# Optimization experiments

Hardware: AMD Instinct MI355X
Metric: run time of the kernel (lower is better)

The kernel has to match this reference:

```python
import jax, jax.numpy as jnp
import numpy as np

B, Q, F, D, H = 16384, 1024, 2, 5, 4  # batch, n_qubits, n_features, depth, heads


def setup_inputs() -> dict:
    key = jax.random.key(0)
    ks = iter(jax.random.split(key, 16))
    def rnd(shape, s=0.02):
        return jax.random.normal(next(ks), shape, dtype=jnp.float32) * s
    return {
        "x": jax.random.normal(next(ks), (B, F), dtype=jnp.float32),
        # amplitude_encoder: Linear(F,4Q) -> LN -> GELU -> Linear(4Q,2Q) -> LN -> Tanh -> Linear(2Q,Q)
        "amp_W1": rnd((4 * Q, F)), "amp_b1": jnp.zeros((4 * Q,), jnp.float32),
        "amp_g1": jnp.ones((4 * Q,), jnp.float32), "amp_be1": jnp.zeros((4 * Q,), jnp.float32),
        "amp_W2": rnd((2 * Q, 4 * Q)), "amp_b2": jnp.zeros((2 * Q,), jnp.float32),
        "amp_g2": jnp.ones((2 * Q,), jnp.float32), "amp_be2": jnp.zeros((2 * Q,), jnp.float32),
        "amp_W3": rnd((Q, 2 * Q)), "amp_b3": jnp.zeros((Q,), jnp.float32),
        # phase_encoder: Linear(F,2Q) -> LN -> SiLU -> Linear(2Q,Q) -> Tanh
        "ph_W1": rnd((2 * Q, F)), "ph_b1": jnp.zeros((2 * Q,), jnp.float32),
        "ph_g1": jnp.ones((2 * Q,), jnp.float32), "ph_be1": jnp.zeros((2 * Q,), jnp.float32),
        "ph_W2": rnd((Q, 2 * Q)), "ph_b2": jnp.zeros((Q,), jnp.float32),
        # rotation parameters (depth, Q, 3); only the last depth slice survives the overwrite loop
        "rot_freq": jax.random.normal(next(ks), (D, Q, 3), dtype=jnp.float32),
        "rot_phase": jax.random.normal(next(ks), (D, Q, 3), dtype=jnp.float32),
        # MultiheadAttention(Q, 4 heads)
        "attn_in_w": rnd((3 * Q, Q)), "attn_in_b": jnp.zeros((3 * Q,), jnp.float32),
        "attn_out_w": rnd((Q, Q)), "attn_out_b": jnp.zeros((Q,), jnp.float32),
    }


def _ln(x, g, b):
    m = jnp.mean(x, -1, keepdims=True)
    v = jnp.mean((x - m) ** 2, -1, keepdims=True)
    return (x - m) * jax.lax.rsqrt(v + 1e-5) * g + b


def reference(x, amp_W1, amp_b1, amp_g1, amp_be1, amp_W2, amp_b2, amp_g2, amp_be2,
              amp_W3, amp_b3, ph_W1, ph_b1, ph_g1, ph_be1, ph_W2, ph_b2,
              rot_freq, rot_phase, attn_in_w, attn_in_b, attn_out_w, attn_out_b):
    # amplitude encoder (Dropout is identity in eval mode)
    h = jax.nn.gelu(_ln(x @ amp_W1.T + amp_b1, amp_g1, amp_be1), approximate=False)
    h = jnp.tanh(_ln(h @ amp_W2.T + amp_b2, amp_g2, amp_be2))
    amp = h @ amp_W3.T + amp_b3                      # (B, Q)
    # phase encoder
    p = jax.nn.silu(_ln(x @ ph_W1.T + ph_b1, ph_g1, ph_be1))
    phase = jnp.tanh(p @ ph_W2.T + ph_b2)            # (B, Q)
    # multiscale conv branch: n_features=2 < min kernel size 3 => skipped, combined_conv = 0
    # depth loop overwrites quantum_state each iteration => only depth index D-1 matters
    rx = jnp.sin(amp * rot_freq[-1, :, 0] + rot_phase[-1, :, 0])
    ry = jnp.cos(phase * rot_freq[-1, :, 1] + rot_phase[-1, :, 1])
    rz = jnp.broadcast_to(jnp.tanh(rot_phase[-1, :, 2]), rx.shape)  # tanh(0*f + p)
    qs = (rx + ry + rz) / 3.0                        # (B, Q)
    # MultiheadAttention with seq_len == 1: softmax over a single key is exactly 1,
    # so attended output == V projection regardless of Q/K.
    qkv = qs @ attn_in_w.T + attn_in_b               # (B, 3Q)
    v = qkv[:, 2 * Q:]                               # (B, Q)
    return v @ attn_out_w.T + attn_out_b
```

## Files before the change

kernel.cpp:

```cpp
#include <hip/hip_runtime.h>

using bf16x8 = __attribute__((ext_vector_type(8))) __bf16;
using u16x8  = __attribute__((ext_vector_type(8))) unsigned short;
using f32x4  = __attribute__((ext_vector_type(4))) float;

__device__ __forceinline__ unsigned short f2bf(float f){
  unsigned int u = __float_as_uint(f);
  u += 0x7fffu + ((u >> 16) & 1u);
  return (unsigned short)(u >> 16);
}
__device__ __forceinline__ float bf2f(unsigned short h){
  return __uint_as_float(((unsigned int)h) << 16);
}

__global__ __launch_bounds__(256) void cvt_bf16(const float* __restrict__ s,
                                                unsigned short* __restrict__ d, int n){
  int i = blockIdx.x * 256 + threadIdx.x;
  if (i < n) d[i] = f2bf(s[i]);
}

__global__ __launch_bounds__(256) void front_amp_kernel(
    const float* __restrict__ x,
    const float* __restrict__ W1, const float* __restrict__ b1,
    const float* __restrict__ g1, const float* __restrict__ be1,
    unsigned short* __restrict__ h)
{
  __shared__ float red[256];
  __shared__ float red2[256];
  __shared__ float s_mean, s_inv;
  const int row = blockIdx.x;
  const int tid = threadIdx.x;
  const float x0 = x[row * 2 + 0];
  const float x1 = x[row * 2 + 1];

  float va[16];
  float sum = 0.f, sq = 0.f;
#pragma unroll
  for (int i = 0; i < 16; i++){
    int j = i * 256 + tid;
    float v = x0 * W1[2 * j] + x1 * W1[2 * j + 1] + b1[j];
    va[i] = v; sum += v; sq += v * v;
  }
  red[tid] = sum; red2[tid] = sq; __syncthreads();
  for (int s = 128; s > 0; s >>= 1){
    if (tid < s){ red[tid] += red[tid + s]; red2[tid] += red2[tid + s]; }
    __syncthreads();
  }
  if (tid == 0){
    float m = red[0] * (1.0f / 4096.0f);
    float v = red2[0] * (1.0f / 4096.0f) - m * m;
    s_mean = m; s_inv = rsqrtf(v + 1e-5f);
  }
  __syncthreads();
  float mean = s_mean, inv = s_inv;
#pragma unroll
  for (int i = 0; i < 16; i++){
    int j = i * 256 + tid;
    float y = (va[i] - mean) * inv * g1[j] + be1[j];
    float ge = 0.5f * y * (1.0f + erff(y * 0.70710678118654752f));
    h[(size_t)row * 4096 + j] = f2bf(ge);
  }
}

__global__ __launch_bounds__(256) void front_ph_kernel(
    const float* __restrict__ x,
    const float* __restrict__ W1, const float* __restrict__ b1,
    const float* __restrict__ g1, const float* __restrict__ be1,
    unsigned short* __restrict__ p)
{
  __shared__ float red[256];
  __shared__ float red2[256];
  __shared__ float s_mean, s_inv;
  const int row = blockIdx.x;
  const int tid = threadIdx.x;
  const float x0 = x[row * 2 + 0];
  const float x1 = x[row * 2 + 1];

  float vp[8];
  float sum = 0.f, sq = 0.f;
#pragma unroll
  for (int i = 0; i < 8; i++){
    int j = i * 256 + tid;
    float v = x0 * W1[2 * j] + x1 * W1[2 * j + 1] + b1[j];
    vp[i] = v; sum += v; sq += v * v;
  }
  red[tid] = sum; red2[tid] = sq; __syncthreads();
  for (int s = 128; s > 0; s >>= 1){
    if (tid < s){ red[tid] += red[tid + s]; red2[tid] += red2[tid + s]; }
    __syncthreads();
  }
  if (tid == 0){
    float m = red[0] * (1.0f / 2048.0f);
    float v = red2[0] * (1.0f / 2048.0f) - m * m;
    s_mean = m; s_inv = rsqrtf(v + 1e-5f);
  }
  __syncthreads();
  float mean = s_mean, inv = s_inv;
#pragma unroll
  for (int i = 0; i < 8; i++){
    int j = i * 256 + tid;
    float y = (vp[i] - mean) * inv * g1[j] + be1[j];
    float si = y / (1.0f + expf(-y));
    p[(size_t)row * 2048 + j] = f2bf(si);
  }
}

__global__ __launch_bounds__(256) void ln_tanh_kernel(
    unsigned short* __restrict__ c, const float* __restrict__ g,
    const float* __restrict__ be)
{
  __shared__ float red[256];
  __shared__ float red2[256];
  __shared__ float s_mean, s_inv;
  const size_t base = (size_t)blockIdx.x * 2048;
  const int tid = threadIdx.x;
  float v[8];
  float sum = 0.f, sq = 0.f;
#pragma unroll
  for (int i = 0; i < 8; i++){
    int j = i * 256 + tid;
    float t = bf2f(c[base + j]);
    v[i] = t; sum += t; sq += t * t;
  }
  red[tid] = sum; red2[tid] = sq; __syncthreads();
  for (int s = 128; s > 0; s >>= 1){
    if (tid < s){ red[tid] += red[tid + s]; red2[tid] += red2[tid + s]; }
    __syncthreads();
  }
  if (tid == 0){
    float m = red[0] * (1.0f / 2048.0f);
    float vv = red2[0] * (1.0f / 2048.0f) - m * m;
    s_mean = m; s_inv = rsqrtf(vv + 1e-5f);
  }
  __syncthreads();
  float mean = s_mean, inv = s_inv;
#pragma unroll
  for (int i = 0; i < 8; i++){
    int j = i * 256 + tid;
    float y = (v[i] - mean) * inv * g[j] + be[j];
    c[base + j] = f2bf(tanhf(y));
  }
}


#define WAITV8() asm volatile("s_waitcnt vmcnt(8)" ::: "memory")
#define WAITV4() asm volatile("s_waitcnt vmcnt(4)" ::: "memory")
#define WAITV0() asm volatile("s_waitcnt vmcnt(0)" ::: "memory")

template<int EPI>
__global__ __launch_bounds__(512, 2) void gemm_bt(
    const unsigned short* __restrict__ A, const unsigned short* __restrict__ B,
    void* __restrict__ outp, int M, int N, int K, int nT,
    const float* __restrict__ bias,
    const float* __restrict__ aux0, const float* __restrict__ aux1,
    const unsigned short* __restrict__ aux2)
{
  __shared__ __align__(16) char smem_raw[131072];
  unsigned short* S = (unsigned short*)smem_raw;

  const int tid  = threadIdx.x;
  const int wave = tid >> 6, lane = tid & 63;
  const int wm = wave >> 1, wn = wave & 1;
  const int lm = lane & 15, lq = lane >> 4;

  int lid = blockIdx.x;
  {
    const int nwg = gridDim.x;
    if ((nwg & 7) == 0) lid = (lid & 7) * (nwg >> 3) + (lid >> 3);
  }
  const int m0 = (lid / nT) * 256, n0 = (lid % nT) * 256;

  f32x4 acc[4][8];
#pragma unroll
  for (int i = 0; i < 4; i++)
#pragma unroll
    for (int j = 0; j < 8; j++) acc[i][j] = (f32x4){0.f, 0.f, 0.f, 0.f};

  const int lr = lane >> 2;
  const int lc = (((lane & 3) ^ ((lr >> 1) & 3)) << 3);
  const unsigned short* gA = A + (size_t)(m0 + wave * 32 + lr) * K + lc;
  const unsigned short* gB = B + (size_t)(n0 + wave * 32 + lr) * K + lc;
  const size_t rowK16 = (size_t)16 * K;

  auto stage = [&](int buf){
    unsigned short* lA = S + buf * 16384 + wave * 1024;
    unsigned short* lB = lA + 8192;
    __builtin_amdgcn_global_load_lds(
        (const __attribute__((address_space(1))) void*)gA,
        (__attribute__((address_space(3))) void*)lA, 16, 0, 0);
    __builtin_amdgcn_global_load_lds(
        (const __attribute__((address_space(1))) void*)(gA + rowK16),
        (__attribute__((address_space(3))) void*)(lA + 512), 16, 0, 0);
    __builtin_amdgcn_global_load_lds(
        (const __attribute__((address_space(1))) void*)gB,
        (__attribute__((address_space(3))) void*)lB, 16, 0, 0);
    __builtin_amdgcn_global_load_lds(
        (const __attribute__((address_space(1))) void*)(gB + rowK16),
        (__attribute__((address_space(3))) void*)(lB + 512), 16, 0, 0);
    gA += 32; gB += 32;
  };

  auto compute = [&](int buf){
    const unsigned short* sA = S + buf * 16384;
    const unsigned short* sB = sA + 8192;
    bf16x8 af[4], bfr[8];
#pragma unroll
    for (int t = 0; t < 4; t++){
      const int r = wm * 64 + t * 16 + lm;
      af[t]  = *(const bf16x8*)&sA[r * 32 + ((lq ^ ((r >> 1) & 3)) << 3)];
    }
#pragma unroll
    for (int t = 0; t < 8; t++){
      const int r = wn * 128 + t * 16 + lm;
      bfr[t] = *(const bf16x8*)&sB[r * 32 + ((lq ^ ((r >> 1) & 3)) << 3)];
    }
    __builtin_amdgcn_s_setprio(1);
#pragma unroll
    for (int i = 0; i < 4; i++)
#pragma unroll
      for (int j = 0; j < 8; j++)
        acc[i][j] = __builtin_amdgcn_mfma_f32_16x16x32_bf16(af[i], bfr[j], acc[i][j], 0, 0, 0);
    __builtin_amdgcn_s_setprio(0);
  };

  const int nTk = K >> 5;
  stage(0); stage(1); stage(2);
  for (int t = 0; t < nTk; ++t){
    if (t + 2 < nTk)      WAITV8();
    else if (t + 1 < nTk) WAITV4();
    else                  WAITV0();
    __builtin_amdgcn_s_barrier();
    if (t + 3 < nTk) stage((t + 3) & 3);
    compute(t & 3);
  }

  __syncthreads();
  float* ew = (float*)smem_raw + wave * 2112;

#pragma unroll
  for (int i = 0; i < 4; i++){
#pragma unroll
    for (int j = 0; j < 8; j++){
      const int col = n0 + wn * 128 + j * 16 + lm;
      float bcol = bias[col];
      float f0 = 0.f, p0 = 0.f, rzv = 0.f;
      if constexpr (EPI == 1){
        f0 = aux0[3 * col]; p0 = aux1[3 * col]; rzv = tanhf(aux1[3 * col + 2]);
      }
      if constexpr (EPI == 2){
        f0 = aux0[3 * col + 1]; p0 = aux1[3 * col + 1];
      }
#pragma unroll
      for (int r = 0; r < 4; r++){
        const float val = acc[i][j][r];
        float pre;
        if constexpr (EPI == 0 || EPI == 3)      pre = val + bcol;
        else if constexpr (EPI == 1)             pre = sinf((val + bcol) * f0 + p0) + rzv;
        else                                     pre = cosf(tanhf(val + bcol) * f0 + p0);
        ew[(lq * 4 + r) * 132 + j * 16 + lm] = pre;
      }
    }
    if constexpr (EPI != 3){
#pragma unroll
      for (int s = 0; s < 4; s++){
        const int lrow = 4 * s + lq;
        const int grow = m0 + wm * 64 + i * 16 + lrow;
        const float* src = ew + lrow * 132 + lm * 8;
        f32x4 v0 = *(const f32x4*)(src);
        f32x4 v1 = *(const f32x4*)(src + 4);
        const size_t gidx = (size_t)grow * N + n0 + wn * 128 + lm * 8;
        u16x8 o;
        if constexpr (EPI == 1){
          u16x8 ry8 = *(const u16x8*)&aux2[gidx];
#pragma unroll
          for (int t = 0; t < 4; t++){
            o[t]     = f2bf((v0[t] + bf2f(ry8[t]))     * (1.0f / 3.0f));
            o[t + 4] = f2bf((v1[t] + bf2f(ry8[t + 4])) * (1.0f / 3.0f));
          }
        } else {
#pragma unroll
          for (int t = 0; t < 4; t++){
            o[t] = f2bf(v0[t]); o[t + 4] = f2bf(v1[t]);
          }
        }
        *(u16x8*)&((unsigned short*)outp)[gidx] = o;
      }
    } else {
#pragma unroll
      for (int s = 0; s < 8; s++){
        const int lrow = 2 * s + (lane >> 5);
        const int grow = m0 + wm * 64 + i * 16 + lrow;
        const int lcol = (lane & 31) * 4;
        f32x4 v = *(const f32x4*)(ew + lrow * 132 + lcol);
        *(f32x4*)&((float*)outp)[(size_t)grow * N + n0 + wn * 128 + lcol] = v;
      }
    }
  }
}

extern "C" void kernel_launch(void* const* d_in, const int* in_sizes, int n_in,
                              void* d_out, int out_size, void* d_ws, size_t ws_size,
                              hipStream_t stream)
{
  const float* x    = (const float*)d_in[0];
  const float* aW1  = (const float*)d_in[1];
  const float* ab1  = (const float*)d_in[2];
  const float* ag1  = (const float*)d_in[3];
  const float* abe1 = (const float*)d_in[4];
  const float* aW2  = (const float*)d_in[5];
  const float* ab2  = (const float*)d_in[6];
  const float* ag2  = (const float*)d_in[7];
  const float* abe2 = (const float*)d_in[8];
  const float* aW3  = (const float*)d_in[9];
  const float* ab3  = (const float*)d_in[10];
  const float* pW1  = (const float*)d_in[11];
  const float* pb1  = (const float*)d_in[12];
  const float* pg1  = (const float*)d_in[13];
  const float* pbe1 = (const float*)d_in[14];
  const float* pW2  = (const float*)d_in[15];
  const float* pb2  = (const float*)d_in[16];
  const float* rfreq  = (const float*)d_in[17];
  const float* rphase = (const float*)d_in[18];
  const float* aiw  = (const float*)d_in[19];
  const float* aib  = (const float*)d_in[20];
  const float* aow  = (const float*)d_in[21];
  const float* aob  = (const float*)d_in[22];

  const int B = 16384, Q = 1024;

  char* ws = (char*)d_ws;
  size_t off = 0;
  auto alloc = [&](size_t bytes) -> char* {
    char* ptr = ws + off; off += (bytes + 255) & ~(size_t)255; return ptr;
  };
  unsigned short* Wb2  = (unsigned short*)alloc((size_t)2 * Q * 4 * Q * 2);
  unsigned short* Wb3  = (unsigned short*)alloc((size_t)Q * 2 * Q * 2);
  unsigned short* PWb2 = (unsigned short*)alloc((size_t)Q * 2 * Q * 2);
  unsigned short* WVb  = (unsigned short*)alloc((size_t)Q * Q * 2);
  unsigned short* WOb  = (unsigned short*)alloc((size_t)Q * Q * 2);
  unsigned short* R1   = (unsigned short*)alloc((size_t)B * 4 * Q * 2);
  unsigned short* ry   = (unsigned short*)alloc((size_t)B * Q * 2);

  unsigned short* p  = R1;
  unsigned short* h  = R1;
  unsigned short* qs = R1;
  unsigned short* v  = R1 + (size_t)B * Q;
  unsigned short* c2 = (unsigned short*)d_out;

  cvt_bf16<<<(2*Q*4*Q + 255) / 256, 256, 0, stream>>>(aW2, Wb2, 2*Q*4*Q);
  cvt_bf16<<<(Q*2*Q + 255) / 256, 256, 0, stream>>>(aW3, Wb3, Q*2*Q);
  cvt_bf16<<<(Q*2*Q + 255) / 256, 256, 0, stream>>>(pW2, PWb2, Q*2*Q);
  cvt_bf16<<<(Q*Q + 255) / 256, 256, 0, stream>>>(aiw + (size_t)2*Q*Q, WVb, Q*Q);
  cvt_bf16<<<(Q*Q + 255) / 256, 256, 0, stream>>>(aow, WOb, Q*Q);

  const float* rf4 = rfreq  + (size_t)4 * Q * 3;
  const float* rp4 = rphase + (size_t)4 * Q * 3;

  const int mT = B / 256;
  const int nT1 = 2 * Q / 256;
  const int nTq = Q / 256;

  front_ph_kernel<<<B, 256, 0, stream>>>(x, pW1, pb1, pg1, pbe1, p);
  gemm_bt<2><<<nTq * mT, 512, 0, stream>>>(p, PWb2, ry, B, Q, 2*Q, nTq,
                                           pb2, rf4, rp4, nullptr);

  front_amp_kernel<<<B, 256, 0, stream>>>(x, aW1, ab1, ag1, abe1, h);
  gemm_bt<0><<<nT1 * mT, 512, 0, stream>>>(h, Wb2, c2, B, 2*Q, 4*Q, nT1,
                                           ab2, nullptr, nullptr, nullptr);
  ln_tanh_kernel<<<B, 256, 0, stream>>>(c2, ag2, abe2);

  gemm_bt<1><<<nTq * mT, 512, 0, stream>>>(c2, Wb3, qs, B, Q, 2*Q, nTq,
                                           ab3, rf4, rp4, ry);
  gemm_bt<0><<<nTq * mT, 512, 0, stream>>>(qs, WVb, v, B, Q, Q, nTq,
                                           aib + 2*Q, nullptr, nullptr, nullptr);
  gemm_bt<3><<<nTq * mT, 512, 0, stream>>>(v, WOb, d_out, B, Q, Q, nTq,
                                           aob, nullptr, nullptr, nullptr);
}
```

Baseline: 848.4 us.

## Vectorize encoder/LN kernels and split GEMM inner step into two barrier-separated halves

The front encoder and LN+tanh kernels switch from strided scalar accesses to contiguous per-thread f32x4 loads and 16-byte bf16 stores, which reduces the number of memory instructions. The GEMM main loop splits each K-step into two phases of 16 MFMAs, with an extra workgroup barrier between them, and reloads the second half of the B fragments. This halves B-fragment register use and is meant to interleave LDS reads with MFMA work across waves. The cost is one extra s_barrier per K-step, which could serialize waves.

Result: slower. 924.2 us (+8.9%).

```diff
diff --git a/kernel.cpp b/kernel.cpp
--- a/kernel.cpp
+++ b/kernel.cpp
@@ -33,13 +33,20 @@
   const float x0 = x[row * 2 + 0];
   const float x1 = x[row * 2 + 1];
 
+  const f32x4* W4 = (const f32x4*)(W1 + (size_t)tid * 32);
   float va[16];
   float sum = 0.f, sq = 0.f;
 #pragma unroll
-  for (int i = 0; i < 16; i++){
-    int j = i * 256 + tid;
-    float v = x0 * W1[2 * j] + x1 * W1[2 * j + 1] + b1[j];
-    va[i] = v; sum += v; sq += v * v;
+  for (int i4 = 0; i4 < 4; i4++){
+    f32x4 b4 = *(const f32x4*)(b1 + tid * 16 + i4 * 4);
+    f32x4 wa = W4[i4 * 2], wb = W4[i4 * 2 + 1];
+    float v0 = x0 * wa[0] + x1 * wa[1] + b4[0];
+    float v1 = x0 * wa[2] + x1 * wa[3] + b4[1];
+    float v2 = x0 * wb[0] + x1 * wb[1] + b4[2];
+    float v3 = x0 * wb[2] + x1 * wb[3] + b4[3];
+    va[i4*4+0] = v0; va[i4*4+1] = v1; va[i4*4+2] = v2; va[i4*4+3] = v3;
+    sum += v0 + v1 + v2 + v3;
+    sq  += v0*v0 + v1*v1 + v2*v2 + v3*v3;
   }
   red[tid] = sum; red2[tid] = sq; __syncthreads();
   for (int s = 128; s > 0; s >>= 1){
@@ -54,11 +61,21 @@
   __syncthreads();
   float mean = s_mean, inv = s_inv;
 #pragma unroll
-  for (int i = 0; i < 16; i++){
-    int j = i * 256 + tid;
-    float y = (va[i] - mean) * inv * g1[j] + be1[j];
-    float ge = 0.5f * y * (1.0f + erff(y * 0.70710678118654752f));
-    h[(size_t)row * 4096 + j] = f2bf(ge);
+  for (int i8 = 0; i8 < 2; i8++){
+    f32x4 ga = *(const f32x4*)(g1  + tid * 16 + i8 * 8);
+    f32x4 gb = *(const f32x4*)(g1  + tid * 16 + i8 * 8 + 4);
+    f32x4 ba = *(const f32x4*)(be1 + tid * 16 + i8 * 8);
+    f32x4 bb = *(const f32x4*)(be1 + tid * 16 + i8 * 8 + 4);
+    u16x8 o;
+#pragma unroll
+    for (int k = 0; k < 8; k++){
+      float gk = (k < 4) ? ga[k] : gb[k - 4];
+      float bk = (k < 4) ? ba[k] : bb[k - 4];
+      float y = (va[i8 * 8 + k] - mean) * inv * gk + bk;
+      float ge = 0.5f * y * (1.0f + erff(y * 0.70710678118654752f));
+      o[k] = f2bf(ge);
+    }
+    *(u16x8*)&h[(size_t)row * 4096 + tid * 16 + i8 * 8] = o;
   }
 }
 
@@ -76,13 +93,20 @@
   const float x0 = x[row * 2 + 0];
   const float x1 = x[row * 2 + 1];
 
+  const f32x4* W4 = (const f32x4*)(W1 + (size_t)tid * 16);
   float vp[8];
   float sum = 0.f, sq = 0.f;
 #pragma unroll
-  for (int i = 0; i < 8; i++){
-    int j = i * 256 + tid;
-    float v = x0 * W1[2 * j] + x1 * W1[2 * j + 1] + b1[j];
-    vp[i] = v; sum += v; sq += v * v;
+  for (int i4 = 0; i4 < 2; i4++){
+    f32x4 b4 = *(const f32x4*)(b1 + tid * 8 + i4 * 4);
+    f32x4 wa = W4[i4 * 2], wb = W4[i4 * 2 + 1];
+    float v0 = x0 * wa[0] + x1 * wa[1] + b4[0];
+    float v1 = x0 * wa[2] + x1 * wa[3] + b4[1];
+    float v2 = x0 * wb[0] + x1 * wb[1] + b4[2];
+    float v3 = x0 * wb[2] + x1 * wb[3] + b4[3];
+    vp[i4*4+0] = v0; vp[i4*4+1] = v1; vp[i4*4+2] = v2; vp[i4*4+3] = v3;
+    sum += v0 + v1 + v2 + v3;
+    sq  += v0*v0 + v1*v1 + v2*v2 + v3*v3;
   }
   red[tid] = sum; red2[tid] = sq; __syncthreads();
   for (int s = 128; s > 0; s >>= 1){
@@ -96,12 +120,21 @@
   }
   __syncthreads();
   float mean = s_mean, inv = s_inv;
-#pragma unroll
-  for (int i = 0; i < 8; i++){
-    int j = i * 256 + tid;
-    float y = (vp[i] - mean) * inv * g1[j] + be1[j];
-    float si = y / (1.0f + expf(-y));
-    p[(size_t)row * 2048 + j] = f2bf(si);
+  {
+    f32x4 ga = *(const f32x4*)(g1  + tid * 8);
+    f32x4 gb = *(const f32x4*)(g1  + tid * 8 + 4);
+    f32x4 ba = *(const f32x4*)(be1 + tid * 8);
+    f32x4 bb = *(const f32x4*)(be1 + tid * 8 + 4);
+    u16x8 o;
+#pragma unroll
+    for (int k = 0; k < 8; k++){
+      float gk = (k < 4) ? ga[k] : gb[k - 4];
+      float bk = (k < 4) ? ba[k] : bb[k - 4];
+      float y = (vp[k] - mean) * inv * gk + bk;
+      float si = y / (1.0f + expf(-y));
+      o[k] = f2bf(si);
+    }
+    *(u16x8*)&p[(size_t)row * 2048 + tid * 8] = o;
   }
 }
 
@@ -114,13 +147,13 @@
   __shared__ float s_mean, s_inv;
   const size_t base = (size_t)blockIdx.x * 2048;
   const int tid = threadIdx.x;
+  u16x8 cv = *(const u16x8*)&c[base + tid * 8];
   float v[8];
   float sum = 0.f, sq = 0.f;
 #pragma unroll
-  for (int i = 0; i < 8; i++){
-    int j = i * 256 + tid;
-    float t = bf2f(c[base + j]);
-    v[i] = t; sum += t; sq += t * t;
+  for (int k = 0; k < 8; k++){
+    float t = bf2f(cv[k]);
+    v[k] = t; sum += t; sq += t * t;
   }
   red[tid] = sum; red2[tid] = sq; __syncthreads();
   for (int s = 128; s > 0; s >>= 1){
@@ -134,11 +167,20 @@
   }
   __syncthreads();
   float mean = s_mean, inv = s_inv;
-#pragma unroll
-  for (int i = 0; i < 8; i++){
-    int j = i * 256 + tid;
-    float y = (v[i] - mean) * inv * g[j] + be[j];
-    c[base + j] = f2bf(tanhf(y));
+  {
+    f32x4 ga = *(const f32x4*)(g  + tid * 8);
+    f32x4 gb = *(const f32x4*)(g  + tid * 8 + 4);
+    f32x4 ba = *(const f32x4*)(be + tid * 8);
+    f32x4 bb = *(const f32x4*)(be + tid * 8 + 4);
+    u16x8 o;
+#pragma unroll
+    for (int k = 0; k < 8; k++){
+      float gk = (k < 4) ? ga[k] : gb[k - 4];
+      float bk = (k < 4) ? ba[k] : bb[k - 4];
+      float y = (v[k] - mean) * inv * gk + bk;
+      o[k] = f2bf(tanhf(y));
+    }
+    *(u16x8*)&c[base + tid * 8] = o;
   }
 }
 
@@ -200,29 +242,6 @@
     gA += 32; gB += 32;
   };
 
-  auto compute = [&](int buf){
-    const unsigned short* sA = S + buf * 16384;
-    const unsigned short* sB = sA + 8192;
-    bf16x8 af[4], bfr[8];
-#pragma unroll
-    for (int t = 0; t < 4; t++){
-      const int r = wm * 64 + t * 16 + lm;
-      af[t]  = *(const bf16x8*)&sA[r * 32 + ((lq ^ ((r >> 1) & 3)) << 3)];
-    }
-#pragma unroll
-    for (int t = 0; t < 8; t++){
-      const int r = wn * 128 + t * 16 + lm;
-      bfr[t] = *(const bf16x8*)&sB[r * 32 + ((lq ^ ((r >> 1) & 3)) << 3)];
-    }
-    __builtin_amdgcn_s_setprio(1);
-#pragma unroll
-    for (int i = 0; i < 4; i++)
-#pragma unroll
-      for (int j = 0; j < 8; j++)
-        acc[i][j] = __builtin_amdgcn_mfma_f32_16x16x32_bf16(af[i], bfr[j], acc[i][j], 0, 0, 0);
-    __builtin_amdgcn_s_setprio(0);
-  };
-
   const int nTk = K >> 5;
   stage(0); stage(1); stage(2);
   for (int t = 0; t < nTk; ++t){
@@ -231,7 +250,43 @@
     else                  WAITV0();
     __builtin_amdgcn_s_barrier();
     if (t + 3 < nTk) stage((t + 3) & 3);
-    compute(t & 3);
+
+    const int buf = t & 3;
+    const unsigned short* sA = S + buf * 16384;
+    const unsigned short* sB = sA + 8192;
+    bf16x8 af[4], bfr[4];
+#pragma unroll
+    for (int q = 0; q < 4; q++){
+      const int r = wm * 64 + q * 16 + lm;
+      af[q] = *(const bf16x8*)&sA[r * 32 + ((lq ^ ((r >> 1) & 3)) << 3)];
+    }
+#pragma unroll
+    for (int q = 0; q < 4; q++){
+      const int r = wn * 128 + q * 16 + lm;
+      bfr[q] = *(const bf16x8*)&sB[r * 32 + ((lq ^ ((r >> 1) & 3)) << 3)];
+    }
+    __builtin_amdgcn_s_setprio(1);
+#pragma unroll
+    for (int i = 0; i < 4; i++)
+#pragma unroll
+      for (int j = 0; j < 4; j++)
+        acc[i][j] = __builtin_amdgcn_mfma_f32_16x16x32_bf16(af[i], bfr[j], acc[i][j], 0, 0, 0);
+    __builtin_amdgcn_s_setprio(0);
+    __builtin_amdgcn_sched_barrier(0);
+    __builtin_amdgcn_s_barrier();
+    __builtin_amdgcn_sched_barrier(0);
+#pragma unroll
+    for (int q = 0; q < 4; q++){
+      const int r = wn * 128 + 64 + q * 16 + lm;
+      bfr[q] = *(const bf16x8*)&sB[r * 32 + ((lq ^ ((r >> 1) & 3)) << 3)];
+    }
+    __builtin_amdgcn_s_setprio(1);
+#pragma unroll
+    for (int i = 0; i < 4; i++)
+#pragma unroll
+      for (int j = 0; j < 4; j++)
+        acc[i][j + 4] = __builtin_amdgcn_mfma_f32_16x16x32_bf16(af[i], bfr[j], acc[i][j + 4], 0, 0, 0);
+    __builtin_amdgcn_s_setprio(0);
   }
 
   __syncthreads();
```
